# Kernel tuning notes

Hardware: AMD Instinct MI355X
Metric: run time of the kernel (lower is better)

Reference implementation:

```python
import math
import jax, jax.numpy as jnp
import numpy as np

EPS_LN = 1e-5
EPS_NORM = 1e-12


def conv2d(x, w, b=None, groups=1):
    # x: (B,C,H,W), w: (O, I//groups, kh, kw)
    out = jax.lax.conv_general_dilated(
        x, w, window_strides=(1, 1), padding='SAME',
        dimension_numbers=('NCHW', 'OIHW', 'NCHW'),
        feature_group_count=groups)
    if b is not None:
        out = out + b[None, :, None, None]
    return out


def layernorm2d(x, w, b):
    # LayerNorm over channel dim of (B,C,H,W)
    mu = x.mean(axis=1, keepdims=True)
    var = ((x - mu) ** 2).mean(axis=1, keepdims=True)
    xn = (x - mu) / jnp.sqrt(var + EPS_LN)
    return xn * w[None, :, None, None] + b[None, :, None, None]


def l2norm(x):
    n = jnp.sqrt((x * x).sum(axis=-1, keepdims=True))
    return x / jnp.maximum(n, EPS_NORM)


def mha(s, Wi, bi, Wo, bo, num_heads):
    # torch nn.MultiheadAttention (batch_first) self-attention
    B, S, C = s.shape
    Dh = C // num_heads
    qkv = s @ Wi.T + bi                      # (B,S,3C)
    q, k, v = jnp.split(qkv, 3, axis=-1)
    hd = lambda t: t.reshape(B, S, num_heads, Dh).transpose(0, 2, 1, 3)
    q, k, v = hd(q), hd(k), hd(v)            # (B,H,S,Dh)
    attn = jax.nn.softmax(jnp.einsum('bhqd,bhkd->bhqk', q, k) / math.sqrt(Dh), axis=-1)
    o = jnp.einsum('bhqk,bhkd->bhqd', attn, v).transpose(0, 2, 1, 3).reshape(B, S, C)
    return o @ Wo.T + bo


def frfn(x, pconv_w, lin1_w, lin1_b, dw_w, dw_b, lin2_w, lin2_b):
    b, c, h, w = x.shape
    dc = c // 4
    x1 = conv2d(x[:, :dc], pconv_w)                       # partial conv, no bias
    x = jnp.concatenate([x1, x[:, dc:]], axis=1)
    xt = x.transpose(0, 2, 3, 1).reshape(b, h * w, c)
    y = jax.nn.gelu(xt @ lin1_w.T + lin1_b, approximate=False)  # (b,hw,2*hid)
    y1, y2 = jnp.split(y, 2, axis=-1)
    hid = lin1_w.shape[0] // 2
    y1 = y1.reshape(b, h, w, hid).transpose(0, 3, 1, 2)
    y1 = jax.nn.gelu(conv2d(y1, dw_w, dw_b, groups=hid), approximate=False)
    y1 = y1.transpose(0, 2, 3, 1).reshape(b, h * w, hid)
    out = (y1 * y2) @ lin2_w.T + lin2_b
    return out.reshape(b, h, w, c).transpose(0, 3, 1, 2)


def setup_inputs() -> dict:
    key = jax.random.key(0)
    ks = jax.random.split(key, 10)
    B, C, H, W = 16, 256, 64, 64
    HID = 2 * C  # FRFN hidden = embed_dim*2
    DC = C // 4
    w = lambda k, shape: (jax.random.normal(k, shape, dtype=jnp.float32) * 0.02)
    return {
        'x': jax.random.normal(ks[0], (B, C, H, W), dtype=jnp.float32),
        'slot_scale': jnp.asarray(C ** -0.5, dtype=jnp.float32),
        'norm1_w': jnp.ones((C,), jnp.float32), 'norm1_b': jnp.zeros((C,), jnp.float32),
        'in_proj_w': w(ks[1], (3 * C, C)), 'in_proj_b': jnp.zeros((3 * C,), jnp.float32),
        'out_proj_w': w(ks[2], (C, C)), 'out_proj_b': jnp.zeros((C,), jnp.float32),
        'norm2_w': jnp.ones((C,), jnp.float32), 'norm2_b': jnp.zeros((C,), jnp.float32),
        'pconv_w': w(ks[3], (DC, DC, 3, 3)),
        'lin1_w': w(ks[4], (2 * HID, C)), 'lin1_b': jnp.zeros((2 * HID,), jnp.float32),
        'dw_w': w(ks[5], (HID, 1, 3, 3)), 'dw_b': jnp.zeros((HID,), jnp.float32),
        'lin2_w': w(ks[6], (C, HID)), 'lin2_b': jnp.zeros((C,), jnp.float32),
    }


def reference(x, slot_scale, norm1_w, norm1_b, in_proj_w, in_proj_b,
              out_proj_w, out_proj_b, norm2_w, norm2_b,
              pconv_w, lin1_w, lin1_b, dw_w, dw_b, lin2_w, lin2_b):
    NUM_HEADS, POOL = 8, 8
    b, c, h, w = x.shape
    copy = x
    # ada_avgpool slot init: 8x8 exact block means (h,w divisible by pool)
    pooled = x.reshape(b, c, POOL, h // POOL, POOL, w // POOL).mean(axis=(3, 5))  # (b,c,8,8)
    init_slots = pooled.transpose(0, 2, 3, 1).reshape(b, POOL * POOL, c)          # (b,S,c)

    shortcut = x
    xn = layernorm2d(x, norm1_w, norm1_b)
    xf = xn.transpose(0, 2, 3, 1).reshape(b, h * w, c)                            # (b,N,c)
    logits = slot_scale * jnp.einsum('bsc,bnc->bsn', l2norm(init_slots), l2norm(xf))
    slots = jnp.einsum('bsn,bnc->bsc', jax.nn.softmax(logits, axis=-1), xf)
    slots = mha(slots, in_proj_w, in_proj_b, out_proj_w, out_proj_b, NUM_HEADS)
    out = jnp.einsum('bns,bsc->bnc', jax.nn.softmax(logits.transpose(0, 2, 1), axis=-1), slots)
    out = out.transpose(0, 2, 1).reshape(b, c, h, w)

    x = shortcut + out
    x = x + frfn(layernorm2d(x, norm2_w, norm2_b),
                 pconv_w, lin1_w, lin1_b, dw_w, dw_b, lin2_w, lin2_b)
    return (x, copy - x)
```

## Files before the change

kernel.cpp:

```cpp
#include <hip/hip_runtime.h>
#include <hip/hip_bf16.h>
#include <stdint.h>
#include <math.h>

#define BB 16
#define CC 256
#define HH 64
#define WW 64
#define NN 4096
#define SS 64
#define NHEAD 8
#define DH 32
#define HID 512
#define DC 64

typedef float    f32x4  __attribute__((ext_vector_type(4)));
typedef uint16_t u16x8  __attribute__((ext_vector_type(8)));
typedef uint16_t u16x4  __attribute__((ext_vector_type(4)));
typedef uint16_t u16x2  __attribute__((ext_vector_type(2)));

__device__ __forceinline__ float gelu_fast(float x){
  float u = 0.7978845608028654f * (x + 0.044715f * x * x * x);
  float e = __expf(2.0f * u);
  float th = 1.0f - 2.0f / (e + 1.0f);
  return 0.5f * x * (1.0f + th);
}
__device__ __forceinline__ uint16_t f2b(float f){
  union { float f; uint32_t u; } v; v.f = f;
  uint32_t r = v.u + 0x7fffu + ((v.u >> 16) & 1u);
  return (uint16_t)(r >> 16);
}
__device__ __forceinline__ float b2f(uint16_t h){
  union { uint32_t u; float f; } v; v.u = ((uint32_t)h) << 16;
  return v.f;
}

__device__ __forceinline__ float waveSum(float v){
#pragma unroll
  for (int m = 32; m >= 1; m >>= 1) v += __shfl_xor(v, m, 64);
  return v;
}
__device__ __forceinline__ float blockSum256(float v, float* s4){
  v = waveSum(v);
  __syncthreads();
  if ((threadIdx.x & 63) == 0) s4[threadIdx.x >> 6] = v;
  __syncthreads();
  return s4[0] + s4[1] + s4[2] + s4[3];
}

__device__ __forceinline__ void g2l16(const void* g, void* l){
  __builtin_amdgcn_global_load_lds((const __attribute__((address_space(1))) uint32_t*)g,
                                   (__attribute__((address_space(3))) uint32_t*)l, 16, 0, 0);
}

__device__ __forceinline__ int swz8(int row, int kp){ return (kp ^ (row & 7)) << 3; }

__device__ __forceinline__ void mfma_bf16(f32x4& d, u16x8 a, u16x8 b){
  asm volatile("v_mfma_f32_16x16x32_bf16 %0, %1, %2, %0" : "+v"(d) : "v"(a), "v"(b));
}

template<int SWA, int SWB>
__device__ __forceinline__ void mma_core(const uint16_t* lA, int lda, const uint16_t* lB, int ldb,
                                         f32x4 (&acc)[4][4], int wrow, int wcol, int lane){
  const int rb = lane & 15, ub = lane >> 4;
#pragma unroll
  for (int ks = 0; ks < 2; ks++){
    const int u = ks * 4 + ub;
    u16x8 af[4], bf[4];
#pragma unroll
    for (int m = 0; m < 4; m++){
      int r = wrow + m * 16 + rb;
      int e = SWA ? ((u ^ (r & 7)) << 3) : (u << 3);
      af[m] = *(const u16x8*)&lA[r * lda + e];
    }
#pragma unroll
    for (int n = 0; n < 4; n++){
      int r = wcol + n * 16 + rb;
      int e = SWB ? ((u ^ (r & 7)) << 3) : (u << 3);
      bf[n] = *(const u16x8*)&lB[r * ldb + e];
    }
#pragma unroll
    for (int m = 0; m < 4; m++)
#pragma unroll
      for (int n = 0; n < 4; n++)
        mfma_bf16(acc[m][n], af[m], bf[n]);
  }
}

__global__ __launch_bounds__(256) void k_t2b(const float* __restrict__ in, uint16_t* __restrict__ out){
  __shared__ float tile[64][33];
  int b = blockIdx.z;
  int n0 = blockIdx.x * 32;
  int c0 = blockIdx.y * 64;
  int tx = threadIdx.x, ty = threadIdx.y;
  const float* src = in + (size_t)b * CC * NN;
#pragma unroll
  for (int i = 0; i < 64; i += 8)
    tile[ty + i][tx] = src[(size_t)(c0 + ty + i) * NN + n0 + tx];
  __syncthreads();
  uint16_t* dst = out + (size_t)b * NN * CC;
#pragma unroll
  for (int i = 0; i < 32; i += 8){
    int r = ty + i;
    u16x2 o; o[0] = f2b(tile[tx * 2][r]); o[1] = f2b(tile[tx * 2 + 1][r]);
    *(u16x2*)&dst[(size_t)(n0 + r) * CC + c0 + tx * 2] = o;
  }
}

__global__ __launch_bounds__(256) void k_pool(const uint16_t* __restrict__ xhwcb, uint16_t* __restrict__ slotsNb){
  int bs = blockIdx.x; int b = bs >> 6, s = bs & 63;
  int sy = (s >> 3) * 8, sx = (s & 7) * 8;
  int t = threadIdx.x;
  int c4 = t & 63, pg = t >> 6;
  const uint16_t* base = xhwcb + (size_t)b * NN * CC;
  float a0 = 0.f, a1 = 0.f, a2 = 0.f, a3 = 0.f;
#pragma unroll
  for (int i = 0; i < 16; i++){
    int p = pg * 16 + i; int py = p >> 3, px = p & 7;
    u16x4 v = *(const u16x4*)&base[(size_t)((sy + py) * WW + sx + px) * CC + c4 * 4];
    a0 += b2f(v[0]); a1 += b2f(v[1]); a2 += b2f(v[2]); a3 += b2f(v[3]);
  }
  __shared__ float sm[4][64][4];
  sm[pg][c4][0] = a0; sm[pg][c4][1] = a1; sm[pg][c4][2] = a2; sm[pg][c4][3] = a3;
  __syncthreads();
  if (t < 64){
    float v0 = (sm[0][t][0] + sm[1][t][0] + sm[2][t][0] + sm[3][t][0]) * (1.0f / 64.0f);
    float v1 = (sm[0][t][1] + sm[1][t][1] + sm[2][t][1] + sm[3][t][1]) * (1.0f / 64.0f);
    float v2 = (sm[0][t][2] + sm[1][t][2] + sm[2][t][2] + sm[3][t][2]) * (1.0f / 64.0f);
    float v3 = (sm[0][t][3] + sm[1][t][3] + sm[2][t][3] + sm[3][t][3]) * (1.0f / 64.0f);
    float ss = waveSum(v0 * v0 + v1 * v1 + v2 * v2 + v3 * v3);
    float inv = 1.0f / fmaxf(sqrtf(ss), 1e-12f);
    u16x4 o; o[0] = f2b(v0 * inv); o[1] = f2b(v1 * inv); o[2] = f2b(v2 * inv); o[3] = f2b(v3 * inv);
    *(u16x4*)&slotsNb[(size_t)bs * CC + t * 4] = o;
  }
}

__global__ __launch_bounds__(256) void k_ln_w(const uint16_t* __restrict__ xa, const uint16_t* __restrict__ xb,
                                              const float* __restrict__ w, const float* __restrict__ b,
                                              uint16_t* __restrict__ xoutb, float* __restrict__ rn,
                                              uint16_t* __restrict__ xn2p){
  int row = blockIdx.x * 4 + (threadIdx.x >> 6);
  int lane = threadIdx.x & 63;
  u16x4 va = *(const u16x4*)&xa[(size_t)row * CC + lane * 4];
  float v0 = b2f(va[0]), v1 = b2f(va[1]), v2 = b2f(va[2]), v3 = b2f(va[3]);
  if (xb){
    u16x4 vb = *(const u16x4*)&xb[(size_t)row * CC + lane * 4];
    v0 += b2f(vb[0]); v1 += b2f(vb[1]); v2 += b2f(vb[2]); v3 += b2f(vb[3]);
  }
  float mu = waveSum(v0 + v1 + v2 + v3) * (1.0f / CC);
  float d0 = v0 - mu, d1 = v1 - mu, d2 = v2 - mu, d3 = v3 - mu;
  float var = waveSum(d0 * d0 + d1 * d1 + d2 * d2 + d3 * d3) * (1.0f / CC);
  float inv = rsqrtf(var + 1e-5f);
  float4 wv = *(const float4*)&w[lane * 4];
  float4 bv = *(const float4*)&b[lane * 4];
  float x0 = d0 * inv * wv.x + bv.x;
  float x1 = d1 * inv * wv.y + bv.y;
  float x2 = d2 * inv * wv.z + bv.z;
  float x3 = d3 * inv * wv.w + bv.w;
  u16x4 o; o[0] = f2b(x0); o[1] = f2b(x1); o[2] = f2b(x2); o[3] = f2b(x3);
  *(u16x4*)&xoutb[(size_t)row * CC + lane * 4] = o;
  if (xn2p && lane < 16){
    int bb = row >> 12, n = row & 4095, y = n >> 6, x = n & 63;
    *(u16x4*)&xn2p[(((size_t)(bb * 66 + y + 1)) * 66 + x + 1) * 64 + lane * 4] = o;
  }
  if (rn){
    float ss = waveSum(x0 * x0 + x1 * x1 + x2 * x2 + x3 * x3);
    if (lane == 0) rn[row] = 1.0f / fmaxf(sqrtf(ss), 1e-12f);
  }
}

__global__ __launch_bounds__(256) void k_zb(uint16_t* __restrict__ xn2p){
  int i = blockIdx.x * 256 + threadIdx.x;
  if (i >= 16 * 260 * 16) return;
  int c4 = i & 15; int rest = i >> 4;
  int j = rest % 260; int b = rest / 260;
  int py, px;
  if (j < 66){ py = 0; px = j; }
  else if (j < 132){ py = 65; px = j - 66; }
  else if (j < 196){ py = j - 132 + 1; px = 0; }
  else { py = j - 196 + 1; px = 65; }
  u16x4 z; z[0] = 0; z[1] = 0; z[2] = 0; z[3] = 0;
  *(u16x4*)&xn2p[(((size_t)(b * 66 + py)) * 66 + px) * 64 + c4 * 4] = z;
}

__global__ __launch_bounds__(256) void k_cvtw(const float* __restrict__ wi, const float* __restrict__ wo,
                                              const float* __restrict__ w1, const float* __restrict__ w2,
                                              const float* __restrict__ pw, const float* __restrict__ dww,
                                              uint16_t* __restrict__ wib, uint16_t* __restrict__ wob,
                                              uint16_t* __restrict__ w1b, uint16_t* __restrict__ w2b,
                                              uint16_t* __restrict__ wp2, float* __restrict__ dwwT){
  int i = blockIdx.x * 256 + threadIdx.x;
  if (i < 163840){
    const float* src; uint16_t* dst; int off;
    if (i < 49152){ src = wi; dst = wib; off = i; }
    else if (i < 65536){ src = wo; dst = wob; off = i - 49152; }
    else if (i < 131072){ src = w1; dst = w1b; off = i - 65536; }
    else { src = w2; dst = w2b; off = i - 131072; }
    float4 v = ((const float4*)src)[off];
    u16x4 o;
    o[0] = f2b(v.x); o[1] = f2b(v.y); o[2] = f2b(v.z); o[3] = f2b(v.w);
    *(u16x4*)&dst[(size_t)off * 4] = o;
  } else if (i < 200704){
    int j = i - 163840;
    if (j < 64 * 576){
      int co = j / 576, r = j % 576, tap = r >> 6, ci = r & 63;
      wp2[j] = f2b(pw[(size_t)co * 576 + ci * 9 + tap]);
    }
  } else {
    int j = i - 200704;
    if (j < 9 * HID){
      int tap = j / HID, ch = j % HID;
      dwwT[j] = dww[(size_t)ch * 9 + tap];
    }
  }
}

__global__ __launch_bounds__(256) void k_logits_mfma(const uint16_t* __restrict__ slotsNb,
                                                     const uint16_t* __restrict__ xnb,
                                                     const float* __restrict__ rn,
                                                     const float* __restrict__ scale_p,
                                                     uint16_t* __restrict__ E){
  __shared__ uint16_t smem[20480];
  __shared__ float rnS[256];
  uint16_t* lA = smem;
  uint16_t* lB = smem + 64 * 64;
  int t = threadIdx.x, lane = t & 63, w = t >> 6;
  int b = blockIdx.y, n0 = blockIdx.x * 256;
  rnS[t] = rn[b * NN + n0 + t];
  f32x4 acc[4][4];
#pragma unroll
  for (int m = 0; m < 4; m++)
#pragma unroll
    for (int n = 0; n < 4; n++) acc[m][n] = (f32x4){0.f, 0.f, 0.f, 0.f};
  for (int kc = 0; kc < 4; kc++){
#pragma unroll
    for (int i = 0; i < 2; i++){
      int idx = i * 256 + t, row = idx >> 3, kp = idx & 7;
      *(u16x8*)&lA[row * 64 + swz8(row, kp)] = *(const u16x8*)&slotsNb[(size_t)(b * 64 + row) * 256 + kc * 64 + kp * 8];
    }
#pragma unroll
    for (int i = 0; i < 8; i++){
      int idx = i * 256 + t, row = idx >> 3, kp = idx & 7;
      *(u16x8*)&lB[row * 64 + swz8(row, kp)] = *(const u16x8*)&xnb[((size_t)b * NN + n0 + row) * 256 + kc * 64 + kp * 8];
    }
    __syncthreads();
    mma_core<1, 1>(lA, 64, lB, 64, acc, 0, w * 64, lane);
    __syncthreads();
  }
  float scale = scale_p[0];
  int rb4 = (lane >> 4) * 4, cb = lane & 15;
#pragma unroll
  for (int m = 0; m < 4; m++)
#pragma unroll
    for (int n = 0; n < 4; n++)
#pragma unroll
      for (int j = 0; j < 4; j++){
        int s = m * 16 + rb4 + j, nl = w * 64 + n * 16 + cb;
        smem[s * 264 + nl] = f2b(__expf(acc[m][n][j] * scale * rnS[nl]));
      }
  __syncthreads();
#pragma unroll
  for (int i = 0; i < 8; i++){
    int idx = i * 256 + t, row = idx >> 5, cseg = idx & 31;
    *(u16x8*)&E[((size_t)b * 64 + row) * NN + n0 + cseg * 8] = *(const u16x8*)&smem[row * 264 + cseg * 8];
  }
}

__global__ __launch_bounds__(256) void k_z1(const uint16_t* __restrict__ E, float* __restrict__ invz1){
  int bs = blockIdx.x, t = threadIdx.x;
  u16x8 v0 = *(const u16x8*)&E[(size_t)bs * NN + t * 16];
  u16x8 v1 = *(const u16x8*)&E[(size_t)bs * NN + t * 16 + 8];
  float s = 0.f;
#pragma unroll
  for (int i = 0; i < 8; i++) s += b2f(v0[i]) + b2f(v1[i]);
  __shared__ float s4[4];
  float z = blockSum256(s, s4);
  if (t == 0) invz1[bs] = 1.0f / z;
}

__global__ __launch_bounds__(256) void k_slots_mfma(const uint16_t* __restrict__ E,
                                                    const uint16_t* __restrict__ xnb,
                                                    float* __restrict__ part){
  __shared__ uint16_t lA[64 * 64];
  __shared__ uint16_t lB[256 * 72];
  int t = threadIdx.x, lane = t & 63, w = t >> 6;
  int ks = blockIdx.x, b = blockIdx.y;
  f32x4 acc[4][4];
#pragma unroll
  for (int m = 0; m < 4; m++)
#pragma unroll
    for (int n = 0; n < 4; n++) acc[m][n] = (f32x4){0.f, 0.f, 0.f, 0.f};
  for (int kc = 0; kc < 8; kc++){
    int n0 = ks * 512 + kc * 64;
#pragma unroll
    for (int i = 0; i < 2; i++){
      int idx = i * 256 + t, row = idx >> 3, kp = idx & 7;
      *(u16x8*)&lA[row * 64 + swz8(row, kp)] = *(const u16x8*)&E[((size_t)b * 64 + row) * NN + n0 + kp * 8];
    }
#pragma unroll
    for (int i = 0; i < 8; i++){
      int idx = i * 256 + t, nrow = idx >> 5, cseg = idx & 31;
      u16x8 v = *(const u16x8*)&xnb[((size_t)b * NN + n0 + nrow) * 256 + cseg * 8];
#pragma unroll
      for (int j = 0; j < 8; j++) lB[(cseg * 8 + j) * 72 + nrow] = v[j];
    }
    __syncthreads();
    mma_core<1, 0>(lA, 64, lB, 72, acc, 0, w * 64, lane);
    __syncthreads();
  }
  int rb4 = (lane >> 4) * 4, cb = lane & 15;
#pragma unroll
  for (int m = 0; m < 4; m++)
#pragma unroll
    for (int n = 0; n < 4; n++)
#pragma unroll
      for (int j = 0; j < 4; j++){
        int s = m * 16 + rb4 + j, c = w * 64 + n * 16 + cb;
        part[(((size_t)b * 8 + ks) * 64 + s) * 256 + c] = acc[m][n][j];
      }
}

__global__ __launch_bounds__(256) void k_fold(const float* __restrict__ part, const float* __restrict__ invz1,
                                              uint16_t* __restrict__ slotsb){
  int i = blockIdx.x * 256 + threadIdx.x;
  int row = i >> 6, c4 = i & 63;
  int b = row >> 6, s = row & 63;
  float4 a = {0.f, 0.f, 0.f, 0.f};
#pragma unroll
  for (int p = 0; p < 8; p++){
    float4 v = *(const float4*)&part[(((size_t)b * 8 + p) * 64 + s) * 256 + c4 * 4];
    a.x += v.x; a.y += v.y; a.z += v.z; a.w += v.w;
  }
  float iz = invz1[row];
  u16x4 o; o[0] = f2b(a.x * iz); o[1] = f2b(a.y * iz); o[2] = f2b(a.z * iz); o[3] = f2b(a.w * iz);
  *(u16x4*)&slotsb[(size_t)row * 256 + c4 * 4] = o;
}

__global__ __launch_bounds__(256) void k_gemm_qkv(const uint16_t* __restrict__ slotsb,
                                                  const uint16_t* __restrict__ wib,
                                                  const float* __restrict__ bi,
                                                  float* __restrict__ qkv){
  __shared__ uint16_t lA[128 * 64];
  __shared__ uint16_t lB[128 * 64];
  int t = threadIdx.x, lane = t & 63, w = t >> 6;
  int wrow = (w >> 1) * 64, wcol = (w & 1) * 64;
  int BR = blockIdx.x * 128, BC = blockIdx.y * 128;
  f32x4 acc[4][4];
#pragma unroll
  for (int m = 0; m < 4; m++)
#pragma unroll
    for (int n = 0; n < 4; n++) acc[m][n] = (f32x4){0.f, 0.f, 0.f, 0.f};
  for (int kc = 0; kc < 4; kc++){
#pragma unroll
    for (int i = 0; i < 4; i++){
      int idx = i * 256 + t, row = idx >> 3, kp = idx & 7;
      *(u16x8*)&lA[row * 64 + swz8(row, kp)] = *(const u16x8*)&slotsb[(size_t)(BR + row) * 256 + kc * 64 + kp * 8];
      *(u16x8*)&lB[row * 64 + swz8(row, kp)] = *(const u16x8*)&wib[(size_t)(BC + row) * 256 + kc * 64 + kp * 8];
    }
    __syncthreads();
    mma_core<1, 1>(lA, 64, lB, 64, acc, wrow, wcol, lane);
    __syncthreads();
  }
  int rb4 = (lane >> 4) * 4, cb = lane & 15;
#pragma unroll
  for (int m = 0; m < 4; m++)
#pragma unroll
    for (int n = 0; n < 4; n++){
      int c = BC + wcol + n * 16 + cb;
      float bias = bi[c];
#pragma unroll
      for (int j = 0; j < 4; j++)
        qkv[(size_t)(BR + wrow + m * 16 + rb4 + j) * 768 + c] = acc[m][n][j] + bias;
    }
}

__global__ __launch_bounds__(256) void k_attn(const float* __restrict__ qkv, uint16_t* __restrict__ aob){
  int b = blockIdx.x >> 3, h = blockIdx.x & 7;
  __shared__ float lq[64][33], lk[64][33], lv[64][33];
  __shared__ float sc[64][65];
  int t = threadIdx.x;
  for (int idx = t; idx < 64 * 32; idx += 256){
    int s = idx >> 5, d = idx & 31;
    const float* base = qkv + ((size_t)b * SS + s) * 768 + h * DH + d;
    lq[s][d] = base[0];
    lk[s][d] = base[256];
    lv[s][d] = base[512];
  }
  __syncthreads();
  const float rs = 0.17677669529663687f;
  for (int idx = t; idx < 64 * 64; idx += 256){
    int qq = idx >> 6, kk = idx & 63;
    float a = 0.f;
#pragma unroll
    for (int d = 0; d < 32; d++) a += lq[qq][d] * lk[kk][d];
    sc[qq][kk] = a * rs;
  }
  __syncthreads();
  {
    int r = t >> 2, sub = t & 3;
    float m = -1e30f;
#pragma unroll
    for (int k = sub * 16; k < sub * 16 + 16; k++) m = fmaxf(m, sc[r][k]);
    m = fmaxf(m, __shfl_xor(m, 1, 64));
    m = fmaxf(m, __shfl_xor(m, 2, 64));
    float z = 0.f;
#pragma unroll
    for (int k = sub * 16; k < sub * 16 + 16; k++){
      float e = __expf(sc[r][k] - m); sc[r][k] = e; z += e;
    }
    z += __shfl_xor(z, 1, 64);
    z += __shfl_xor(z, 2, 64);
    float iv = 1.0f / z;
#pragma unroll
    for (int k = sub * 16; k < sub * 16 + 16; k++) sc[r][k] *= iv;
  }
  __syncthreads();
  for (int idx = t; idx < 64 * 32; idx += 256){
    int qq = idx >> 5, d = idx & 31;
    float a = 0.f;
#pragma unroll
    for (int k = 0; k < 64; k++) a += sc[qq][k] * lv[k][d];
    aob[((size_t)b * SS + qq) * CC + h * DH + d] = f2b(a);
  }
}

__global__ __launch_bounds__(256) void k_gemm_oproj(const uint16_t* __restrict__ aob,
                                                    const uint16_t* __restrict__ wob,
                                                    const float* __restrict__ bo,
                                                    uint16_t* __restrict__ sl2Tb){
  __shared__ uint16_t lA[128 * 64];
  __shared__ uint16_t lB[128 * 64];
  int t = threadIdx.x, lane = t & 63, w = t >> 6;
  int wrow = (w >> 1) * 64, wcol = (w & 1) * 64;
  int BR = blockIdx.x * 128, BC = blockIdx.y * 128;
  f32x4 acc[4][4];
#pragma unroll
  for (int m = 0; m < 4; m++)
#pragma unroll
    for (int n = 0; n < 4; n++) acc[m][n] = (f32x4){0.f, 0.f, 0.f, 0.f};
  for (int kc = 0; kc < 4; kc++){
#pragma unroll
    for (int i = 0; i < 4; i++){
      int idx = i * 256 + t, row = idx >> 3, kp = idx & 7;
      *(u16x8*)&lA[row * 64 + swz8(row, kp)] = *(const u16x8*)&aob[(size_t)(BR + row) * 256 + kc * 64 + kp * 8];
      *(u16x8*)&lB[row * 64 + swz8(row, kp)] = *(const u16x8*)&wob[(size_t)(BC + row) * 256 + kc * 64 + kp * 8];
    }
    __syncthreads();
    mma_core<1, 1>(lA, 64, lB, 64, acc, wrow, wcol, lane);
    __syncthreads();
  }
  int rb4 = (lane >> 4) * 4, cb = lane & 15;
#pragma unroll
  for (int m = 0; m < 4; m++)
#pragma unroll
    for (int n = 0; n < 4; n++){
      int c = BC + wcol + n * 16 + cb;
      float bias = bo[c];
#pragma unroll
      for (int j = 0; j < 4; j++){
        int r = BR + wrow + m * 16 + rb4 + j;
        int b = r >> 6, s = r & 63;
        sl2Tb[((size_t)b * 256 + c) * 64 + s] = f2b(acc[m][n][j] + bias);
      }
    }
}

__global__ __launch_bounds__(256) void k_mix(const uint16_t* __restrict__ E, const uint16_t* __restrict__ sl2Tb,
                                             uint16_t* __restrict__ mixb){
  __shared__ uint16_t lA[128 * 72];
  __shared__ uint16_t lB[128 * 64];
  __shared__ float z2S[128];
  int t = threadIdx.x, lane = t & 63, w = t >> 6;
  int wrow = (w >> 1) * 64, wcol = (w & 1) * 64;
  int BR = blockIdx.x * 128, BC = blockIdx.y * 128, b = blockIdx.z;
#pragma unroll
  for (int i = 0; i < 4; i++){
    int idx = i * 256 + t; int s = idx >> 4, n8 = (idx & 15) * 8;
    u16x8 v = *(const u16x8*)&E[((size_t)b * 64 + s) * NN + BR + n8];
#pragma unroll
    for (int j = 0; j < 8; j++) lA[(n8 + j) * 72 + s] = v[j];
  }
#pragma unroll
  for (int i = 0; i < 4; i++){
    int idx = i * 256 + t, row = idx >> 3, kp = idx & 7;
    *(u16x8*)&lB[row * 64 + swz8(row, kp)] = *(const u16x8*)&sl2Tb[((size_t)b * 256 + BC + row) * 64 + kp * 8];
  }
  __syncthreads();
  if (t < 128){
    float s = 0.f;
#pragma unroll
    for (int k2 = 0; k2 < 64; k2++) s += b2f(lA[t * 72 + k2]);
    z2S[t] = 1.0f / s;
  }
  __syncthreads();
  f32x4 acc[4][4];
#pragma unroll
  for (int m = 0; m < 4; m++)
#pragma unroll
    for (int n = 0; n < 4; n++) acc[m][n] = (f32x4){0.f, 0.f, 0.f, 0.f};
  mma_core<0, 1>(lA, 72, lB, 64, acc, wrow, wcol, lane);
  int rb4 = (lane >> 4) * 4, cb = lane & 15;
#pragma unroll
  for (int m = 0; m < 4; m++)
#pragma unroll
    for (int n = 0; n < 4; n++)
#pragma unroll
      for (int j = 0; j < 4; j++){
        int lrow = wrow + m * 16 + rb4 + j;
        size_t gi = ((size_t)b * NN + BR + lrow) * 256 + BC + wcol + n * 16 + cb;
        mixb[gi] = f2b(acc[m][n][j] * z2S[lrow]);
      }
}

__global__ __launch_bounds__(256) void k_pconv_mfma(const uint16_t* __restrict__ xn2p,
                                                    const uint16_t* __restrict__ wp2,
                                                    uint16_t* __restrict__ pcb){
  __shared__ uint16_t lA[256 * 64];
  __shared__ uint16_t lB[64 * 64];
  int t = threadIdx.x, lane = t & 63, w = t >> 6;
  int wrow = w * 64;
  int BR = blockIdx.x * 256;
  f32x4 acc[4][4];
#pragma unroll
  for (int m = 0; m < 4; m++)
#pragma unroll
    for (int n = 0; n < 4; n++) acc[m][n] = (f32x4){0.f, 0.f, 0.f, 0.f};
  for (int tap = 0; tap < 9; tap++){
    int dy = tap / 3 - 1, dx = tap % 3 - 1;
#pragma unroll
    for (int i = 0; i < 8; i++){
      int q = (w * 8 + i) * 64 + lane;
      int row = q >> 3, kpe = swz8(row, q & 7);
      int r = BR + row;
      int b = r >> 12, n = r & 4095, y = n >> 6, x = n & 63;
      size_t p = ((size_t)(b * 66 + (y + 1 + dy)) * 66 + (x + 1 + dx)) * 64 + kpe;
      g2l16(&xn2p[p], &lA[(w * 8 + i) * 512]);
    }
#pragma unroll
    for (int i = 0; i < 2; i++){
      int q = (w * 2 + i) * 64 + lane;
      int row = q >> 3, kpe = swz8(row, q & 7);
      g2l16(&wp2[(size_t)row * 576 + tap * 64 + kpe], &lB[(w * 2 + i) * 512]);
    }
    __syncthreads();
    mma_core<1, 1>(lA, 64, lB, 64, acc, wrow, 0, lane);
    __syncthreads();
  }
  int rb4 = (lane >> 4) * 4, cb = lane & 15;
#pragma unroll
  for (int m = 0; m < 4; m++)
#pragma unroll
    for (int n = 0; n < 4; n++)
#pragma unroll
      for (int j = 0; j < 4; j++)
        pcb[(size_t)(BR + wrow + m * 16 + rb4 + j) * 64 + (n * 16 + cb)] = f2b(acc[m][n][j]);
}

__global__ __launch_bounds__(512) void k_lin1_mfma(const uint16_t* __restrict__ pcb,
                                                   const uint16_t* __restrict__ xn2b,
                                                   const uint16_t* __restrict__ w1b,
                                                   const float* __restrict__ b1,
                                                   uint16_t* __restrict__ Y1b, uint16_t* __restrict__ Y2b){
  __shared__ uint16_t lA[256 * 64];
  __shared__ uint16_t lB[128 * 64];
  int t = threadIdx.x, lane = t & 63, w = t >> 6;
  int wrow = (w >> 1) * 64, wcol = (w & 1) * 64;
  int bid = blockIdx.x;
  int xcd = bid & 7, i5 = bid >> 3;
  int BR = (xcd * 32 + (i5 >> 3)) * 256;
  int BC = (i5 & 7) * 128;
  f32x4 acc[4][4];
#pragma unroll
  for (int m = 0; m < 4; m++)
#pragma unroll
    for (int n = 0; n < 4; n++) acc[m][n] = (f32x4){0.f, 0.f, 0.f, 0.f};
  for (int kc = 0; kc < 4; kc++){
#pragma unroll
    for (int i = 0; i < 4; i++){
      int q = (w * 4 + i) * 64 + lane;
      int row = q >> 3, kpe = swz8(row, q & 7);
      size_t gr = (size_t)(BR + row);
      const uint16_t* src = (kc == 0) ? &pcb[gr * 64 + kpe] : &xn2b[gr * 256 + kc * 64 + kpe];
      g2l16(src, &lA[(w * 4 + i) * 512]);
    }
#pragma unroll
    for (int i = 0; i < 2; i++){
      int q = (w * 2 + i) * 64 + lane;
      int row = q >> 3, kpe = swz8(row, q & 7);
      g2l16(&w1b[(size_t)(BC + row) * 256 + kc * 64 + kpe], &lB[(w * 2 + i) * 512]);
    }
    __syncthreads();
    mma_core<1, 1>(lA, 64, lB, 64, acc, wrow, wcol, lane);
    __syncthreads();
  }
  int rb4 = (lane >> 4) * 4, cb = lane & 15;
#pragma unroll
  for (int m = 0; m < 4; m++){
#pragma unroll
    for (int n = 0; n < 4; n++){
      int c = BC + wcol + n * 16 + cb;
      float bias = b1[c];
#pragma unroll
      for (int j = 0; j < 4; j++){
        size_t r = (size_t)(BR + wrow + m * 16 + rb4 + j);
        uint16_t h = f2b(gelu_fast(acc[m][n][j] + bias));
        if (c < HID) Y1b[r * HID + c] = h;
        else         Y2b[r * HID + (c - HID)] = h;
      }
    }
  }
}

__global__ __launch_bounds__(256) void k_dwconv(const uint16_t* __restrict__ Y1b,
                                                const float* __restrict__ dwwT,
                                                const float* __restrict__ dwb,
                                                const uint16_t* __restrict__ Y2b,
                                                uint16_t* __restrict__ YPb){
  __shared__ uint16_t lds[3 * 18 * 136];
  int b = blockIdx.z, chunk = blockIdx.y;
  int y = blockIdx.x >> 2, seg = blockIdx.x & 3;
  int x0 = seg * 16;
  int t = threadIdx.x;
  const uint16_t* base = Y1b + (size_t)b * NN * HID + chunk * 128;
  const u16x8 z = {0, 0, 0, 0, 0, 0, 0, 0};
#pragma unroll
  for (int i = 0; i < 4; i++){
    int idx = i * 256 + t;
    if (idx < 864){
      int g8 = idx & 15, rest = idx >> 4;
      int c = rest % 18, r = rest / 18;
      int ry = y + r - 1, xx = x0 + c - 1;
      u16x8 v = z;
      if (ry >= 0 && ry < HH && xx >= 0 && xx < WW)
        v = *(const u16x8*)&base[(size_t)(ry * WW + xx) * HID + g8 * 8];
      *(u16x8*)&lds[(r * 18 + c) * 136 + g8 * 8] = v;
    }
  }
  __syncthreads();
  int px = t >> 4, g8 = t & 15;
  int cg = chunk * 128 + g8 * 8;
  int n = y * WW + x0 + px;
  u16x8 y2 = *(const u16x8*)&Y2b[((size_t)b * NN + n) * HID + cg];
  float acc[8];
  {
    float4 b0 = *(const float4*)&dwb[cg];
    float4 b1 = *(const float4*)&dwb[cg + 4];
    acc[0] = b0.x; acc[1] = b0.y; acc[2] = b0.z; acc[3] = b0.w;
    acc[4] = b1.x; acc[5] = b1.y; acc[6] = b1.z; acc[7] = b1.w;
  }
#pragma unroll
  for (int r = 0; r < 3; r++)
#pragma unroll
    for (int dx = 0; dx < 3; dx++){
      u16x8 v = *(const u16x8*)&lds[(r * 18 + px + dx) * 136 + g8 * 8];
      const float* wt = &dwwT[(r * 3 + dx) * HID + cg];
      float4 w0 = *(const float4*)wt;
      float4 w1 = *(const float4*)(wt + 4);
      acc[0] += b2f(v[0]) * w0.x; acc[1] += b2f(v[1]) * w0.y;
      acc[2] += b2f(v[2]) * w0.z; acc[3] += b2f(v[3]) * w0.w;
      acc[4] += b2f(v[4]) * w1.x; acc[5] += b2f(v[5]) * w1.y;
      acc[6] += b2f(v[6]) * w1.z; acc[7] += b2f(v[7]) * w1.w;
    }
  u16x8 o;
#pragma unroll
  for (int j = 0; j < 8; j++) o[j] = f2b(gelu_fast(acc[j]) * b2f(y2[j]));
  *(u16x8*)&YPb[((size_t)b * NN + n) * HID + cg] = o;
}

__global__ __launch_bounds__(512) void k_lin2_mfma(const uint16_t* __restrict__ YPb,
                                                   const uint16_t* __restrict__ w2b,
                                                   const float* __restrict__ b2,
                                                   uint16_t* __restrict__ deltab){
  __shared__ uint16_t lA[256 * 64];
  __shared__ uint16_t lB[128 * 64];
  int t = threadIdx.x, lane = t & 63, w = t >> 6;
  int wrow = (w >> 1) * 64, wcol = (w & 1) * 64;
  int bid = blockIdx.x;
  int xcd = bid & 7, i5 = bid >> 3;
  int BR = (xcd * 32 + (i5 >> 1)) * 256;
  int BC = (i5 & 1) * 128;
  f32x4 acc[4][4];
#pragma unroll
  for (int m = 0; m < 4; m++)
#pragma unroll
    for (int n = 0; n < 4; n++) acc[m][n] = (f32x4){0.f, 0.f, 0.f, 0.f};
  for (int kc = 0; kc < 8; kc++){
#pragma unroll
    for (int i = 0; i < 4; i++){
      int q = (w * 4 + i) * 64 + lane;
      int row = q >> 3, kpe = swz8(row, q & 7);
      g2l16(&YPb[(size_t)(BR + row) * HID + kc * 64 + kpe], &lA[(w * 4 + i) * 512]);
    }
#pragma unroll
    for (int i = 0; i < 2; i++){
      int q = (w * 2 + i) * 64 + lane;
      int row = q >> 3, kpe = swz8(row, q & 7);
      g2l16(&w2b[(size_t)(BC + row) * HID + kc * 64 + kpe], &lB[(w * 2 + i) * 512]);
    }
    __syncthreads();
    mma_core<1, 1>(lA, 64, lB, 64, acc, wrow, wcol, lane);
    __syncthreads();
  }
  int rb4 = (lane >> 4) * 4, cb = lane & 15;
#pragma unroll
  for (int m = 0; m < 4; m++){
#pragma unroll
    for (int n = 0; n < 4; n++){
      int c = BC + wcol + n * 16 + cb;
      float bias = b2[c];
#pragma unroll
      for (int j = 0; j < 4; j++){
        size_t gr = (size_t)(BR + wrow + m * 16 + rb4 + j);
        deltab[gr * CC + c] = f2b(acc[m][n][j] + bias);
      }
    }
  }
}

__global__ __launch_bounds__(256) void k_final2(const uint16_t* __restrict__ mixb,
                                                const uint16_t* __restrict__ deltab,
                                                const uint16_t* __restrict__ xhwcb,
                                                float* __restrict__ out){
  __shared__ float t0[64 * 68];
  __shared__ float t1[64 * 68];
  int b = blockIdx.z;
  int n0 = blockIdx.x * 64, c0 = blockIdx.y * 64;
  int t = threadIdx.x;
#pragma unroll
  for (int i = 0; i < 4; i++){
    int idx = i * 256 + t, row = idx >> 4, c4 = idx & 15;
    size_t gp = ((size_t)b * NN + n0 + row) * CC + c0 + c4 * 4;
    u16x4 m = *(const u16x4*)&mixb[gp];
    u16x4 d = *(const u16x4*)&deltab[gp];
    u16x4 xh = *(const u16x4*)&xhwcb[gp];
    f32x4 v0, v1;
#pragma unroll
    for (int j = 0; j < 4; j++){
      float v = b2f(m[j]) + b2f(d[j]);
      v0[j] = b2f(xh[j]) + v;
      v1[j] = -v;
    }
    *(f32x4*)&t0[row * 68 + c4 * 4] = v0;
    *(f32x4*)&t1[row * 68 + c4 * 4] = v1;
  }
  __syncthreads();
  int cl = t >> 2, seg = t & 3;
  float* o1 = out + (size_t)BB * CC * NN;
  size_t gbase = ((size_t)(b * CC + c0 + cl)) * NN + n0 + seg * 16;
#pragma unroll
  for (int k = 0; k < 4; k++){
    float4 a, c;
    a.x = t0[(seg * 16 + k * 4 + 0) * 68 + cl];
    a.y = t0[(seg * 16 + k * 4 + 1) * 68 + cl];
    a.z = t0[(seg * 16 + k * 4 + 2) * 68 + cl];
    a.w = t0[(seg * 16 + k * 4 + 3) * 68 + cl];
    c.x = t1[(seg * 16 + k * 4 + 0) * 68 + cl];
    c.y = t1[(seg * 16 + k * 4 + 1) * 68 + cl];
    c.z = t1[(seg * 16 + k * 4 + 2) * 68 + cl];
    c.w = t1[(seg * 16 + k * 4 + 3) * 68 + cl];
    *(float4*)&out[gbase + k * 4] = a;
    *(float4*)&o1[gbase + k * 4] = c;
  }
}

extern "C" void kernel_launch(void* const* d_in, const int* in_sizes, int n_in,
                              void* d_out, int out_size, void* d_ws, size_t ws_size,
                              hipStream_t stream){
  const float* x       = (const float*)d_in[0];
  const float* scale_p = (const float*)d_in[1];
  const float* n1w     = (const float*)d_in[2];
  const float* n1b     = (const float*)d_in[3];
  const float* wi      = (const float*)d_in[4];
  const float* bi      = (const float*)d_in[5];
  const float* wo      = (const float*)d_in[6];
  const float* bo      = (const float*)d_in[7];
  const float* n2w     = (const float*)d_in[8];
  const float* n2b     = (const float*)d_in[9];
  const float* pw      = (const float*)d_in[10];
  const float* w1      = (const float*)d_in[11];
  const float* b1      = (const float*)d_in[12];
  const float* dww     = (const float*)d_in[13];
  const float* dwb     = (const float*)d_in[14];
  const float* w2      = (const float*)d_in[15];
  const float* b2      = (const float*)d_in[16];

  float* base = (float*)d_ws;
  size_t off = 0;
  float* part = base + off; off += (size_t)BB * 8 * SS * CC;
  float* QKV  = base + off; off += (size_t)BB * SS * 3 * CC;
  float* RN   = base + off; off += (size_t)BB * NN;
  float* IZ1  = base + off; off += (size_t)BB * SS;
  float* dwwT = base + off; off += (size_t)9 * HID;
  uint16_t* slotsNb = (uint16_t*)(base + off); off += (size_t)BB * SS * CC / 2;
  uint16_t* slotsb  = (uint16_t*)(base + off); off += (size_t)BB * SS * CC / 2;
  uint16_t* aob     = (uint16_t*)(base + off); off += (size_t)BB * SS * CC / 2;
  uint16_t* sl2Tb   = (uint16_t*)(base + off); off += (size_t)BB * CC * SS / 2;
  uint16_t* xhwcb   = (uint16_t*)(base + off); off += (size_t)BB * NN * CC / 2;
  uint16_t* xnb     = (uint16_t*)(base + off); off += (size_t)BB * NN * CC / 2;
  uint16_t* mixb    = (uint16_t*)(base + off); off += (size_t)BB * NN * CC / 2;
  uint16_t* deltab  = (uint16_t*)(base + off); off += (size_t)BB * NN * CC / 2;
  uint16_t* E       = (uint16_t*)(base + off); off += (size_t)BB * SS * NN / 2;
  uint16_t* w1b     = (uint16_t*)(base + off); off += (size_t)(2 * HID) * CC / 2;
  uint16_t* w2b     = (uint16_t*)(base + off); off += (size_t)CC * HID / 2;
  uint16_t* wib     = (uint16_t*)(base + off); off += (size_t)(3 * CC) * CC / 2;
  uint16_t* wob     = (uint16_t*)(base + off); off += (size_t)CC * CC / 2;
  uint16_t* wp2     = (uint16_t*)(base + off); off += (size_t)64 * 576 / 2 + 16;
  uint16_t* Y1b     = (uint16_t*)(base + off); off += (size_t)BB * NN * HID / 2;
  uint16_t* Y2b     = (uint16_t*)(base + off); off += (size_t)BB * NN * HID / 2;
  uint16_t* YPb     = (uint16_t*)(base + off); off += (size_t)BB * NN * HID / 2;
  uint16_t* xn2b    = (uint16_t*)(base + off); off += (size_t)BB * NN * CC / 2;
  uint16_t* xn2p    = (uint16_t*)(base + off); off += (size_t)BB * 66 * 66 * 64 / 2;
  uint16_t* pcb     = (uint16_t*)(base + off); off += (size_t)BB * NN * 64 / 2;
  if (ws_size < off * sizeof(float)) return;
  float* OUT = (float*)d_out;

  dim3 tb2(32, 8);
  k_t2b<<<dim3(NN / 32, CC / 64, BB), tb2, 0, stream>>>(x, xhwcb);
  k_pool<<<BB * SS, 256, 0, stream>>>(xhwcb, slotsNb);
  k_ln_w<<<BB * NN / 4, 256, 0, stream>>>(xhwcb, (const uint16_t*)nullptr, n1w, n1b, xnb, RN,
                                          (uint16_t*)nullptr);
  k_cvtw<<<803, 256, 0, stream>>>(wi, wo, w1, w2, pw, dww, wib, wob, w1b, w2b, wp2, dwwT);
  k_zb<<<(16 * 260 * 16 + 255) / 256, 256, 0, stream>>>(xn2p);
  k_logits_mfma<<<dim3(NN / 256, BB), 256, 0, stream>>>(slotsNb, xnb, RN, scale_p, E);
  k_z1<<<BB * SS, 256, 0, stream>>>(E, IZ1);
  k_slots_mfma<<<dim3(8, BB), 256, 0, stream>>>(E, xnb, part);
  k_fold<<<(BB * SS * CC / 4) / 256, 256, 0, stream>>>(part, IZ1, slotsb);
  k_gemm_qkv<<<dim3(8, 6), 256, 0, stream>>>(slotsb, wib, bi, QKV);
  k_attn<<<BB * NHEAD, 256, 0, stream>>>(QKV, aob);
  k_gemm_oproj<<<dim3(8, 2), 256, 0, stream>>>(aob, wob, bo, sl2Tb);
  k_mix<<<dim3(NN / 128, CC / 128, BB), 256, 0, stream>>>(E, sl2Tb, mixb);
  k_ln_w<<<BB * NN / 4, 256, 0, stream>>>(xhwcb, mixb, n2w, n2b, xn2b, (float*)nullptr, xn2p);
  k_pconv_mfma<<<BB * NN / 256, 256, 0, stream>>>(xn2p, wp2, pcb);
  k_lin1_mfma<<<2048, 512, 0, stream>>>(pcb, xn2b, w1b, b1, Y1b, Y2b);
  k_dwconv<<<dim3(256, 4, BB), 256, 0, stream>>>(Y1b, dwwT, dwb, Y2b, YPb);
  k_lin2_mfma<<<512, 512, 0, stream>>>(YPb, w2b, b2, deltab);
  k_final2<<<dim3(NN / 64, CC / 64, BB), 256, 0, stream>>>(mixb, deltab, xhwcb, OUT);
}
```

Before: 465.8 us.

## Load lin1/lin2 weight fragments directly from global; halve slots split-K

In the lin1 and lin2 GEMMs, the B (weight) tile is no longer staged through shared memory. Each wave reads its MFMA B fragments straight from global memory, relying on cache since the weights are small and shared across blocks, and LDS use per block drops. Separately, the slots GEMM split-K factor goes from 8 to 4, which halves the partial-sum writes and the fold reads but launches fewer blocks (64) with longer loops. The global fragment loads are uncoalesced 16-byte reads that may add latency inside the MFMA loop.

After: 614.4 us. +31.9%, slower.

```diff
diff --git a/kernel.cpp b/kernel.cpp
--- a/kernel.cpp
+++ b/kernel.cpp
@@ -290,8 +290,8 @@
   for (int m = 0; m < 4; m++)
 #pragma unroll
     for (int n = 0; n < 4; n++) acc[m][n] = (f32x4){0.f, 0.f, 0.f, 0.f};
-  for (int kc = 0; kc < 8; kc++){
-    int n0 = ks * 512 + kc * 64;
+  for (int kc = 0; kc < 16; kc++){
+    int n0 = ks * 1024 + kc * 64;
 #pragma unroll
     for (int i = 0; i < 2; i++){
       int idx = i * 256 + t, row = idx >> 3, kp = idx & 7;
@@ -316,7 +316,7 @@
 #pragma unroll
       for (int j = 0; j < 4; j++){
         int s = m * 16 + rb4 + j, c = w * 64 + n * 16 + cb;
-        part[(((size_t)b * 8 + ks) * 64 + s) * 256 + c] = acc[m][n][j];
+        part[(((size_t)b * 4 + ks) * 64 + s) * 256 + c] = acc[m][n][j];
       }
 }
 
@@ -327,8 +327,8 @@
   int b = row >> 6, s = row & 63;
   float4 a = {0.f, 0.f, 0.f, 0.f};
 #pragma unroll
-  for (int p = 0; p < 8; p++){
-    float4 v = *(const float4*)&part[(((size_t)b * 8 + p) * 64 + s) * 256 + c4 * 4];
+  for (int p = 0; p < 4; p++){
+    float4 v = *(const float4*)&part[(((size_t)b * 4 + p) * 64 + s) * 256 + c4 * 4];
     a.x += v.x; a.y += v.y; a.z += v.z; a.w += v.w;
   }
   float iz = invz1[row];
@@ -562,13 +562,13 @@
                                                    const float* __restrict__ b1,
                                                    uint16_t* __restrict__ Y1b, uint16_t* __restrict__ Y2b){
   __shared__ uint16_t lA[256 * 64];
-  __shared__ uint16_t lB[128 * 64];
   int t = threadIdx.x, lane = t & 63, w = t >> 6;
   int wrow = (w >> 1) * 64, wcol = (w & 1) * 64;
   int bid = blockIdx.x;
   int xcd = bid & 7, i5 = bid >> 3;
   int BR = (xcd * 32 + (i5 >> 3)) * 256;
   int BC = (i5 & 7) * 128;
+  const int rb = lane & 15, ub = lane >> 4;
   f32x4 acc[4][4];
 #pragma unroll
   for (int m = 0; m < 4; m++)
@@ -583,14 +583,25 @@
       const uint16_t* src = (kc == 0) ? &pcb[gr * 64 + kpe] : &xn2b[gr * 256 + kc * 64 + kpe];
       g2l16(src, &lA[(w * 4 + i) * 512]);
     }
-#pragma unroll
-    for (int i = 0; i < 2; i++){
-      int q = (w * 2 + i) * 64 + lane;
-      int row = q >> 3, kpe = swz8(row, q & 7);
-      g2l16(&w1b[(size_t)(BC + row) * 256 + kc * 64 + kpe], &lB[(w * 2 + i) * 512]);
-    }
-    __syncthreads();
-    mma_core<1, 1>(lA, 64, lB, 64, acc, wrow, wcol, lane);
+    __syncthreads();
+#pragma unroll
+    for (int ks = 0; ks < 2; ks++){
+      const int u = ks * 4 + ub;
+      u16x8 af[4], bf[4];
+#pragma unroll
+      for (int m = 0; m < 4; m++){
+        int r = wrow + m * 16 + rb;
+        af[m] = *(const u16x8*)&lA[r * 64 + ((u ^ (r & 7)) << 3)];
+      }
+#pragma unroll
+      for (int n = 0; n < 4; n++)
+        bf[n] = *(const u16x8*)&w1b[(size_t)(BC + wcol + n * 16 + rb) * 256 + kc * 64 + u * 8];
+#pragma unroll
+      for (int m = 0; m < 4; m++)
+#pragma unroll
+        for (int n = 0; n < 4; n++)
+          mfma_bf16(acc[m][n], af[m], bf[n]);
+    }
     __syncthreads();
   }
   int rb4 = (lane >> 4) * 4, cb = lane & 15;
@@ -672,13 +683,13 @@
                                                    const float* __restrict__ b2,
                                                    uint16_t* __restrict__ deltab){
   __shared__ uint16_t lA[256 * 64];
-  __shared__ uint16_t lB[128 * 64];
   int t = threadIdx.x, lane = t & 63, w = t >> 6;
   int wrow = (w >> 1) * 64, wcol = (w & 1) * 64;
   int bid = blockIdx.x;
   int xcd = bid & 7, i5 = bid >> 3;
   int BR = (xcd * 32 + (i5 >> 1)) * 256;
   int BC = (i5 & 1) * 128;
+  const int rb = lane & 15, ub = lane >> 4;
   f32x4 acc[4][4];
 #pragma unroll
   for (int m = 0; m < 4; m++)
@@ -691,14 +702,25 @@
       int row = q >> 3, kpe = swz8(row, q & 7);
       g2l16(&YPb[(size_t)(BR + row) * HID + kc * 64 + kpe], &lA[(w * 4 + i) * 512]);
     }
-#pragma unroll
-    for (int i = 0; i < 2; i++){
-      int q = (w * 2 + i) * 64 + lane;
-      int row = q >> 3, kpe = swz8(row, q & 7);
-      g2l16(&w2b[(size_t)(BC + row) * HID + kc * 64 + kpe], &lB[(w * 2 + i) * 512]);
-    }
-    __syncthreads();
-    mma_core<1, 1>(lA, 64, lB, 64, acc, wrow, wcol, lane);
+    __syncthreads();
+#pragma unroll
+    for (int ks = 0; ks < 2; ks++){
+      const int u = ks * 4 + ub;
+      u16x8 af[4], bf[4];
+#pragma unroll
+      for (int m = 0; m < 4; m++){
+        int r = wrow + m * 16 + rb;
+        af[m] = *(const u16x8*)&lA[r * 64 + ((u ^ (r & 7)) << 3)];
+      }
+#pragma unroll
+      for (int n = 0; n < 4; n++)
+        bf[n] = *(const u16x8*)&w2b[(size_t)(BC + wcol + n * 16 + rb) * 512 + kc * 64 + u * 8];
+#pragma unroll
+      for (int m = 0; m < 4; m++)
+#pragma unroll
+        for (int n = 0; n < 4; n++)
+          mfma_bf16(acc[m][n], af[m], bf[n]);
+    }
     __syncthreads();
   }
   int rb4 = (lane >> 4) * 4, cb = lane & 15;
@@ -823,7 +845,7 @@
   k_zb<<<(16 * 260 * 16 + 255) / 256, 256, 0, stream>>>(xn2p);
   k_logits_mfma<<<dim3(NN / 256, BB), 256, 0, stream>>>(slotsNb, xnb, RN, scale_p, E);
   k_z1<<<BB * SS, 256, 0, stream>>>(E, IZ1);
-  k_slots_mfma<<<dim3(8, BB), 256, 0, stream>>>(E, xnb, part);
+  k_slots_mfma<<<dim3(4, BB), 256, 0, stream>>>(E, xnb, part);
   k_fold<<<(BB * SS * CC / 4) / 256, 256, 0, stream>>>(part, IZ1, slotsb);
   k_gemm_qkv<<<dim3(8, 6), 256, 0, stream>>>(slotsb, wib, bi, QKV);
   k_attn<<<BB * NHEAD, 256, 0, stream>>>(QKV, aob);
```
